# Kernel tuning notes

Hardware: AMD Instinct MI355X
Metric: run time of the kernel (lower is better)

The kernel has to match this reference:

```python
import jax, jax.numpy as jnp
import numpy as np

B, L, H = 32, 4096, 1024

def setup_inputs() -> dict:
    key = jax.random.key(0)
    k1, k2, k3 = jax.random.split(key, 3)
    hidden = jax.random.normal(k1, (1, B, H), dtype=jnp.float32)
    encoder_outputs = jax.random.normal(k2, (L, B, H), dtype=jnp.float32)
    W = jax.random.normal(k3, (H, H), dtype=jnp.float32) / np.sqrt(H)
    b = jnp.zeros((H,), dtype=jnp.float32)
    return {"hidden": hidden, "encoder_outputs": encoder_outputs, "W": W, "b": b}

def reference(hidden, encoder_outputs, W, b):
    # Luong 'general' attention: energy[b,i] = hidden[b] . (W @ enc[i,b] + bias)
    # attn(encoder_output): Linear(H, H) -> enc @ W.T + b
    proj = jnp.einsum('lbh,gh->lbg', encoder_outputs, W) + b  # [L,B,H]
    hid = hidden[0]                                            # [B,H]
    energies = jnp.einsum('bh,lbh->bl', hid, proj)             # [B,L]
    attn = jax.nn.softmax(energies, axis=-1)                   # softmax over time
    return attn[:, None, :]                                    # [B,1,L]
```

## Files before the change

kernel.cpp:

```cpp
#include <hip/hip_runtime.h>
#include <math.h>

#define Bsz 32
#define Lsz 4096
#define Hsz 1024

__global__ __launch_bounds__(256) void proj_hidden_k(const float* __restrict__ hid,
                                                     const float* __restrict__ W,
                                                     float* __restrict__ v) {
    const int h = blockIdx.x * 256 + threadIdx.x;
    const int b = blockIdx.y;
    const float* hb = hid + b * Hsz;
    float acc = 0.f;
#pragma unroll 8
    for (int g = 0; g < Hsz; ++g) {
        acc += hb[g] * W[g * Hsz + h];
    }
    v[b * Hsz + h] = acc;
}

__global__ __launch_bounds__(256) void energies_k(const float* __restrict__ enc,
                                                  const float* __restrict__ v,
                                                  float* __restrict__ energy) {
    const int lane = threadIdx.x & 63;
    const int wid  = blockIdx.x * 4 + (threadIdx.x >> 6);
    const int b  = wid >> 7;
    const int l0 = (wid & 127) * 32;

    const float4* v4 = (const float4*)(v + b * Hsz);
    float4 vf[4];
#pragma unroll
    for (int k = 0; k < 4; ++k) vf[k] = v4[k * 64 + lane];

    float res = 0.f;
#pragma unroll 4
    for (int r = 0; r < 32; ++r) {
        const int l = l0 + r;
        const float4* row = (const float4*)(enc + ((size_t)l * Bsz + b) * Hsz);
        float p = 0.f;
#pragma unroll
        for (int k = 0; k < 4; ++k) {
            float4 e = row[k * 64 + lane];
            p += e.x * vf[k].x + e.y * vf[k].y + e.z * vf[k].z + e.w * vf[k].w;
        }
#pragma unroll
        for (int off = 32; off > 0; off >>= 1)
            p += __shfl_xor(p, off, 64);
        if (lane == r) res = p;
    }
    if (lane < 32) energy[b * Lsz + l0 + lane] = res;
}

__global__ __launch_bounds__(256) void softmax_k(const float* __restrict__ energy,
                                                 float* __restrict__ out) {
    __shared__ float smax[4], ssum[4];
    const int b = blockIdx.x;
    const int tid = threadIdx.x;
    const int lane = tid & 63, w = tid >> 6;
    const float4* row = (const float4*)(energy + b * Lsz);
    float4 e[4];
#pragma unroll
    for (int k = 0; k < 4; ++k) e[k] = row[k * 256 + tid];

    float m = -INFINITY;
#pragma unroll
    for (int k = 0; k < 4; ++k)
        m = fmaxf(m, fmaxf(fmaxf(e[k].x, e[k].y), fmaxf(e[k].z, e[k].w)));
#pragma unroll
    for (int off = 32; off > 0; off >>= 1) m = fmaxf(m, __shfl_xor(m, off, 64));
    if (lane == 0) smax[w] = m;
    __syncthreads();
    m = fmaxf(fmaxf(smax[0], smax[1]), fmaxf(smax[2], smax[3]));

    float s = 0.f;
#pragma unroll
    for (int k = 0; k < 4; ++k) {
        e[k].x = __expf(e[k].x - m); e[k].y = __expf(e[k].y - m);
        e[k].z = __expf(e[k].z - m); e[k].w = __expf(e[k].w - m);
        s += e[k].x + e[k].y + e[k].z + e[k].w;
    }
#pragma unroll
    for (int off = 32; off > 0; off >>= 1) s += __shfl_xor(s, off, 64);
    if (lane == 0) ssum[w] = s;
    __syncthreads();
    s = ssum[0] + ssum[1] + ssum[2] + ssum[3];
    const float inv = 1.f / s;

    float4* o = (float4*)(out + b * Lsz);
#pragma unroll
    for (int k = 0; k < 4; ++k) {
        float4 r = e[k];
        r.x *= inv; r.y *= inv; r.z *= inv; r.w *= inv;
        o[k * 256 + tid] = r;
    }
}

extern "C" void kernel_launch(void* const* d_in, const int* in_sizes, int n_in,
                              void* d_out, int out_size, void* d_ws, size_t ws_size,
                              hipStream_t stream) {
    const float* hid = (const float*)d_in[0];
    const float* enc = (const float*)d_in[1];
    const float* W   = (const float*)d_in[2];
    float* out = (float*)d_out;

    float* v      = (float*)d_ws;
    float* energy = v + Bsz * Hsz;

    proj_hidden_k<<<dim3(Hsz / 256, Bsz), 256, 0, stream>>>(hid, W, v);
    energies_k<<<dim3((Lsz * Bsz) / (4 * 32)), 256, 0, stream>>>(enc, v, energy);
    softmax_k<<<dim3(Bsz), 256, 0, stream>>>(energy, out);
}
```

Baseline: 749.6 us.

## Split-K the hidden projection and use a transpose-style butterfly reduction for energies

The hidden-projection kernel now splits the 1024-long reduction across four wavefronts per block and combines the partials in shared memory, launching four times as many blocks for better occupancy. The energies kernel stores all 32 row partial dot products in registers and reduces them together with a recursive-halving butterfly exchange instead of a full 6-step shuffle reduction per row, which cuts the shuffle count substantially. The butterfly leaves results in bit-permuted lane order, so the output row index is remapped. This raises register pressure from the 32-element array, and the main cost, streaming 512MB of encoder outputs, is unchanged.

```diff
diff --git a/kernel.cpp b/kernel.cpp
--- a/kernel.cpp
+++ b/kernel.cpp
@@ -8,15 +8,21 @@
 __global__ __launch_bounds__(256) void proj_hidden_k(const float* __restrict__ hid,
                                                      const float* __restrict__ W,
                                                      float* __restrict__ v) {
-    const int h = blockIdx.x * 256 + threadIdx.x;
+    __shared__ float red[256];
+    const int hl    = threadIdx.x & 63;
+    const int chunk = threadIdx.x >> 6;
+    const int h = blockIdx.x * 64 + hl;
     const int b = blockIdx.y;
-    const float* hb = hid + b * Hsz;
+    const float* hb = hid + b * Hsz + chunk * 256;
+    const float* Wp = W + (size_t)(chunk * 256) * Hsz + h;
     float acc = 0.f;
 #pragma unroll 8
-    for (int g = 0; g < Hsz; ++g) {
-        acc += hb[g] * W[g * Hsz + h];
-    }
-    v[b * Hsz + h] = acc;
+    for (int g = 0; g < 256; ++g)
+        acc += hb[g] * Wp[(size_t)g * Hsz];
+    red[threadIdx.x] = acc;
+    __syncthreads();
+    if (chunk == 0)
+        v[b * Hsz + h] = red[hl] + red[hl + 64] + red[hl + 128] + red[hl + 192];
 }
 
 __global__ __launch_bounds__(256) void energies_k(const float* __restrict__ enc,
@@ -32,23 +38,40 @@
 #pragma unroll
     for (int k = 0; k < 4; ++k) vf[k] = v4[k * 64 + lane];
 
-    float res = 0.f;
+    float vals[32];
 #pragma unroll 4
     for (int r = 0; r < 32; ++r) {
-        const int l = l0 + r;
-        const float4* row = (const float4*)(enc + ((size_t)l * Bsz + b) * Hsz);
+        const float4* row = (const float4*)(enc + ((size_t)(l0 + r) * Bsz + b) * Hsz);
         float p = 0.f;
 #pragma unroll
         for (int k = 0; k < 4; ++k) {
             float4 e = row[k * 64 + lane];
             p += e.x * vf[k].x + e.y * vf[k].y + e.z * vf[k].z + e.w * vf[k].w;
         }
+        vals[r] = p;
+    }
+
+    int cnt = 32;
 #pragma unroll
-        for (int off = 32; off > 0; off >>= 1)
-            p += __shfl_xor(p, off, 64);
-        if (lane == r) res = p;
+    for (int p = 0; p < 5; ++p) {
+        const int m = 1 << p;
+        const int half = cnt >> 1;
+        const bool hi = (lane & m) != 0;
+#pragma unroll
+        for (int j = 0; j < half; ++j) {
+            float send = hi ? vals[j] : vals[half + j];
+            float recv = __shfl_xor(send, m, 64);
+            vals[j] = (hi ? vals[half + j] : vals[j]) + recv;
+        }
+        cnt = half;
     }
-    if (lane < 32) energy[b * Lsz + l0 + lane] = res;
+    float tot = vals[0] + __shfl_xor(vals[0], 32, 64);
+
+    if (lane < 32) {
+        const int row = ((lane & 1) << 4) | ((lane & 2) << 2) | (lane & 4) |
+                        ((lane & 8) >> 2) | ((lane & 16) >> 4);
+        energy[b * Lsz + l0 + row] = tot;
+    }
 }
 
 __global__ __launch_bounds__(256) void softmax_k(const float* __restrict__ energy,
@@ -106,7 +129,7 @@
     float* v      = (float*)d_ws;
     float* energy = v + Bsz * Hsz;
 
-    proj_hidden_k<<<dim3(Hsz / 256, Bsz), 256, 0, stream>>>(hid, W, v);
+    proj_hidden_k<<<dim3(Hsz / 64, Bsz), 256, 0, stream>>>(hid, W, v);
     energies_k<<<dim3((Lsz * Bsz) / (4 * 32)), 256, 0, stream>>>(enc, v, energy);
     softmax_k<<<dim3(Bsz), 256, 0, stream>>>(energy, out);
 }
```

After: 721.9 us. 1.04x faster.
